# Performance work log

Hardware: AMD Instinct MI355X
Metric: run time of the kernel (lower is better)

Reference implementation:

```python
import jax, jax.numpy as jnp
import numpy as np
import math

HIDDEN = 1024
HEADS = 16
HEAD_DIM = HIDDEN // HEADS
B, S = 2, 2048


def setup_inputs() -> dict:
    key = jax.random.key(0)
    ks = jax.random.split(key, 10)
    std = 1.0 / math.sqrt(HIDDEN)
    mk = lambda k: (jax.random.normal(k, (HIDDEN, HIDDEN), jnp.float32) * std)
    return {
        "hidden_states": jax.random.normal(ks[0], (B, S, HIDDEN), jnp.float32),
        "attention_mask": jnp.zeros((B, 1, 1, S), jnp.float32),
        "wq": mk(ks[1]), "bq": jnp.zeros((HIDDEN,), jnp.float32),
        "wk": mk(ks[2]), "bk": jnp.zeros((HIDDEN,), jnp.float32),
        "wv": mk(ks[3]), "bv": jnp.zeros((HIDDEN,), jnp.float32),
        "wo": mk(ks[4]), "bo": jnp.zeros((HIDDEN,), jnp.float32),
    }


def reference(hidden_states, attention_mask, wq, bq, wk, bk, wv, bv, wo, bo):
    b, s, _ = hidden_states.shape
    scale = math.sqrt(HEAD_DIM)
    # projections (torch Linear: x @ W.T + b); weights stored as [out, in]
    q = hidden_states @ wq.T + bq
    k = hidden_states @ wk.T + bk
    v = hidden_states @ wv.T + bv
    # [B, H, S, D]
    q = q.reshape(b, s, HEADS, HEAD_DIM).transpose(0, 2, 1, 3)
    k = k.reshape(b, s, HEADS, HEAD_DIM).transpose(0, 2, 1, 3)
    v = v.reshape(b, s, HEADS, HEAD_DIM).transpose(0, 2, 1, 3)
    scores = jnp.einsum("bhqd,bhkd->bhqk", q, k) / scale
    scores = scores + attention_mask  # broadcast [B,1,1,S]
    weights = jax.nn.softmax(scores, axis=-1)  # dropout = identity (eval)
    out = jnp.einsum("bhqk,bhkd->bhqd", weights, v)
    out = out.transpose(0, 2, 1, 3).reshape(b, s, HIDDEN)
    out = out @ wo.T + bo
    return out
```

## Files before the change

### kernel.cpp

```cpp
#include <hip/hip_runtime.h>
#include <hip/hip_bf16.h>

typedef __bf16 bf16_t;
typedef __bf16 bf16x8 __attribute__((ext_vector_type(8)));
typedef _Float16 f16x4 __attribute__((ext_vector_type(4)));
typedef _Float16 f16x8 __attribute__((ext_vector_type(8)));
typedef float f32x4 __attribute__((ext_vector_type(4)));

#define SEQ    2048
#define NH     16
#define HD     64
#define HIDDEN 1024
#define LOG2E  1.44269504f
#define CSTR   41

#if __has_builtin(__builtin_amdgcn_exp2f)
#define EXP2F(x) __builtin_amdgcn_exp2f(x)
#else
#define EXP2F(x) exp2f(x)
#endif

__device__ __forceinline__ bf16_t to_bf16(float f) { return (bf16_t)f; }

__device__ __forceinline__ void async16(const void* g, void* l) {
    __builtin_amdgcn_global_load_lds((const __attribute__((address_space(1))) void*)g,
                                     (__attribute__((address_space(3))) void*)l, 16, 0, 0);
}

__global__ __launch_bounds__(256) void cvt_kernel(
    const float* __restrict__ s0, bf16_t* __restrict__ d0, int c0,
    const float* __restrict__ s1, bf16_t* __restrict__ d1, int c1,
    const float* __restrict__ s2, bf16_t* __restrict__ d2, int c2,
    const float* __restrict__ s3, bf16_t* __restrict__ d3, int c3,
    const float* __restrict__ s4, bf16_t* __restrict__ d4, int c4,
    const float* __restrict__ s5, float* __restrict__ d5)
{
    int blk = blockIdx.x;
    const float* s; bf16_t* d;
    if (blk < c0)              { s = s0; d = d0; }
    else if ((blk -= c0) < c1) { s = s1; d = d1; }
    else if ((blk -= c1) < c2) { s = s2; d = d2; }
    else if ((blk -= c2) < c3) { s = s3; d = d3; }
    else if ((blk -= c3) < c4) { s = s4; d = d4; }
    else {
        blk -= c4;
        const size_t base = (size_t)blk * 2048 + threadIdx.x * 8;
        float4 a = *(const float4*)&s5[base];
        float4 b = *(const float4*)&s5[base + 4];
        a.x *= LOG2E; a.y *= LOG2E; a.z *= LOG2E; a.w *= LOG2E;
        b.x *= LOG2E; b.y *= LOG2E; b.z *= LOG2E; b.w *= LOG2E;
        *(float4*)&d5[base] = a;
        *(float4*)&d5[base + 4] = b;
        return;
    }
    const size_t base = (size_t)blk * 2048 + threadIdx.x * 8;
    const float4 a = *(const float4*)&s[base];
    const float4 b = *(const float4*)&s[base + 4];
    bf16x8 o;
    o[0] = (bf16_t)a.x; o[1] = (bf16_t)a.y; o[2] = (bf16_t)a.z; o[3] = (bf16_t)a.w;
    o[4] = (bf16_t)b.x; o[5] = (bf16_t)b.y; o[6] = (bf16_t)b.z; o[7] = (bf16_t)b.w;
    *(bf16x8*)&d[base] = o;
}

__global__ __launch_bounds__(256, 3) void qkv_kernel(
    const bf16_t* __restrict__ X,
    const bf16_t* __restrict__ wq, const bf16_t* __restrict__ wk, const bf16_t* __restrict__ wv,
    const float* __restrict__ bq, const float* __restrict__ bk, const float* __restrict__ bv,
    bf16_t* __restrict__ qws, bf16_t* __restrict__ kws, _Float16* __restrict__ vws)
{
    __shared__ __align__(16) bf16_t Sh[16384];
    const int z = blockIdx.z;
    const bf16_t* Wsel = (z == 0) ? wq : (z == 1) ? wk : wv;
    const float*  bsel = (z == 0) ? bq : (z == 1) ? bk : bv;
    const int m0 = blockIdx.y * 128, n0 = blockIdx.x * 128;

    const int t = threadIdx.x, lane = t & 63, w = t >> 6;
    const int w0 = w & 1, w1 = w >> 1, l15 = lane & 15, q4 = lane >> 4;

    f32x4 acc[4][4];
#pragma unroll
    for (int i = 0; i < 4; i++)
#pragma unroll
        for (int j = 0; j < 4; j++) acc[i][j] = f32x4{0.f, 0.f, 0.f, 0.f};

    auto stage = [&](int kt, int buf) {
#pragma unroll
        for (int j = 0; j < 2; j++) {
            const int s = j * 256 + t;
            const int row = s >> 2, c = (s & 3) ^ (row & 3);
            const int lb = buf * 8192 + (j * 256 + w * 64) * 8;
            async16(&X[(size_t)(m0 + row) * HIDDEN + kt + c * 8], &Sh[lb]);
            async16(&Wsel[(size_t)(n0 + row) * HIDDEN + kt + c * 8], &Sh[lb + 4096]);
        }
    };
    stage(0, 0);

    for (int it = 0; it < 32; it++) {
        const int cur = it & 1;
        __syncthreads();
        if (it < 31) stage((it + 1) * 32, cur ^ 1);
        const bf16_t* As = &Sh[cur * 8192];
        const bf16_t* Bs = &Sh[cur * 8192 + 4096];
        bf16x8 af[4];
#pragma unroll
        for (int ti = 0; ti < 4; ti++) {
            const int ra = w0 * 64 + ti * 16 + l15;
            af[ti] = *(const bf16x8*)&As[ra * 32 + (q4 ^ (ra & 3)) * 8];
        }
#pragma unroll
        for (int tj = 0; tj < 4; tj++) {
            const int rb = w1 * 64 + tj * 16 + l15;
            const bf16x8 bfr = *(const bf16x8*)&Bs[rb * 32 + (q4 ^ (rb & 3)) * 8];
#pragma unroll
            for (int ti = 0; ti < 4; ti++)
                acc[ti][tj] = __builtin_amdgcn_mfma_f32_16x16x32_bf16(af[ti], bfr, acc[ti][tj], 0, 0, 0);
        }
    }
    __syncthreads();

    if (z < 2) {
#pragma unroll
        for (int tj = 0; tj < 4; tj++) {
            const int n = w1 * 64 + tj * 16 + l15;
            const float bb = bsel[n0 + n];
            const int ch = (n >> 3), sub = n & 7;
#pragma unroll
            for (int ti = 0; ti < 4; ti++)
#pragma unroll
                for (int r = 0; r < 4; r++) {
                    const int m = w0 * 64 + ti * 16 + q4 * 4 + r;
                    Sh[m * 128 + ((ch ^ (m & 15)) << 3) + sub] = to_bf16(acc[ti][tj][r] + bb);
                }
        }
        __syncthreads();
        bf16_t* dst = (z == 0) ? qws : kws;
#pragma unroll
        for (int i = 0; i < 8; i++) {
            const int g = i * 256 + t;
            const int row = g >> 4, c = g & 15;
            const bf16x8 vv = *(const bf16x8*)&Sh[row * 128 + ((c ^ (row & 15)) << 3)];
            *(bf16x8*)&dst[(size_t)(m0 + row) * HIDDEN + n0 + c * 8] = vv;
        }
    } else {
        _Float16* Vt = (_Float16*)Sh;
#pragma unroll
        for (int tj = 0; tj < 4; tj++) {
            const int n = w1 * 64 + tj * 16 + l15;
            const float bb = bsel[n0 + n];
#pragma unroll
            for (int ti = 0; ti < 4; ti++) {
                const int mb = w0 * 64 + ti * 16 + q4 * 4;
                f16x4 v;
#pragma unroll
                for (int r = 0; r < 4; r++) v[r] = (_Float16)(acc[ti][tj][r] + bb);
                *(f16x4*)&Vt[n * 128 + (((mb >> 3) ^ (n & 15)) << 3) + (mb & 7)] = v;
            }
        }
        __syncthreads();
        const int b = m0 >> 11, sbase = m0 & (SEQ - 1);
#pragma unroll
        for (int i = 0; i < 8; i++) {
            const int g = i * 256 + t;
            const int row = g >> 4, c = g & 15;
            const int sA = (c >> 2) * 32 + (c & 3) * 4;
            const int sB = sA + 16;
            const f16x4 va = *(const f16x4*)&Vt[row * 128 + (((sA >> 3) ^ (row & 15)) << 3) + (sA & 7)];
            const f16x4 vb = *(const f16x4*)&Vt[row * 128 + (((sB >> 3) ^ (row & 15)) << 3) + (sB & 7)];
            f16x8 vv;
            vv[0] = va[0]; vv[1] = va[1]; vv[2] = va[2]; vv[3] = va[3];
            vv[4] = vb[0]; vv[5] = vb[1]; vv[6] = vb[2]; vv[7] = vb[3];
            const int d = (n0 + row) & 63, hh = (n0 + row) >> 6;
            *(f16x8*)&vws[(((size_t)b * NH + hh) * HD + d) * SEQ + sbase + c * 8] = vv;
        }
    }
}

__global__ __launch_bounds__(256, 4) void attn_kernel(
    const bf16_t* __restrict__ Qw, const bf16_t* __restrict__ Kw,
    const _Float16* __restrict__ Vtw, const float* __restrict__ Msc,
    bf16_t* __restrict__ Ow)
{
    __shared__ __align__(16) bf16_t Tiles[2][2][64 * 64];

    const int t = threadIdx.x, lane = t & 63, w = t >> 6;
    const int l15 = lane & 15, q4 = lane >> 4;
    const int wq = w & 1, kp = w >> 1;
    const int lid = blockIdx.x;
    const int c8 = lid & 7, jx = lid >> 3;
    const int bh = c8 * 4 + (jx >> 5);
    const int q0 = (jx & 31) * 64;
    const int b = bh >> 4, h = bh & 15;

    const bf16_t* Qh = Qw + (size_t)b * SEQ * HIDDEN + h * HD;
    const bf16_t* Kh = Kw + (size_t)b * SEQ * HIDDEN + h * HD;
    const _Float16* Vh = Vtw + (size_t)bh * HD * SEQ;
    const float* Mrow = Msc + (size_t)b * SEQ;

    bf16x8 qf[2][2];
#pragma unroll
    for (int qb = 0; qb < 2; qb++)
#pragma unroll
        for (int ks = 0; ks < 2; ks++)
            qf[qb][ks] = *(const bf16x8*)&Qh[(size_t)(q0 + wq * 32 + qb * 16 + l15) * HIDDEN + ks * 32 + q4 * 8];

    f32x4 oacc[2][4];
#pragma unroll
    for (int qb = 0; qb < 2; qb++)
#pragma unroll
        for (int db = 0; db < 4; db++) oacc[qb][db] = f32x4{0.f, 0.f, 0.f, 0.f};
    f32x4 osum[2];
    osum[0] = f32x4{0.f, 0.f, 0.f, 0.f};
    osum[1] = f32x4{0.f, 0.f, 0.f, 0.f};

    f16x8 vone;
#pragma unroll
    for (int i = 0; i < 8; i++) vone[i] = (_Float16)1.0f;

    int koff[4];
#pragma unroll
    for (int cb = 0; cb < 2; cb++)
#pragma unroll
        for (int ks = 0; ks < 2; ks++) {
            const int rk = kp * 32 + cb * 16 + l15;
            koff[cb * 2 + ks] = rk * 64 + (((ks * 4 + q4) ^ (rk & 7)) << 3);
        }
    int voff[4];
#pragma unroll
    for (int db = 0; db < 4; db++) {
        const int rv = db * 16 + l15;
        voff[db] = rv * 64 + (((kp * 4 + q4) ^ (rv & 7)) << 3);
    }

    const int rs0 = t >> 3, cs0 = (t & 7) ^ (rs0 & 7);
    const int rs1 = 32 + rs0, cs1 = (t & 7) ^ (rs1 & 7);
    const bf16_t*   Kp0 = Kh + (size_t)rs0 * HIDDEN + cs0 * 8;
    const bf16_t*   Kp1 = Kh + (size_t)rs1 * HIDDEN + cs1 * 8;
    const _Float16* Vp0 = Vh + (size_t)rs0 * SEQ + cs0 * 8;
    const _Float16* Vp1 = Vh + (size_t)rs1 * SEQ + cs1 * 8;
    const int db0 = (0 * 256 + w * 64) * 8, db1 = (1 * 256 + w * 64) * 8;

    auto stageKV = [&](int it, int buf) {
        const int kt = it * 64;
        bf16_t*   Kd = &Tiles[buf][0][0];
        _Float16* Vd = (_Float16*)&Tiles[buf][1][0];
        async16(Kp0 + (size_t)kt * HIDDEN, &Kd[db0]);
        async16(Vp0 + kt,                  &Vd[db0]);
        async16(Kp1 + (size_t)kt * HIDDEN, &Kd[db1]);
        async16(Vp1 + kt,                  &Vd[db1]);
    };

    auto iterBody = [&](int it, int buf) {
        __syncthreads();
        if (it < 31) stageKV(it + 1, buf ^ 1);

        const bf16_t*   Ksh = &Tiles[buf][0][0];
        const _Float16* Vsh = (const _Float16*)&Tiles[buf][1][0];

        float4 mv4[2];
#pragma unroll
        for (int cb = 0; cb < 2; cb++)
            mv4[cb] = *(const float4*)&Mrow[it * 64 + kp * 32 + cb * 16 + q4 * 4];

        f32x4 sa[2][2];
#pragma unroll
        for (int qb = 0; qb < 2; qb++)
#pragma unroll
            for (int cb = 0; cb < 2; cb++) sa[qb][cb] = f32x4{0.f, 0.f, 0.f, 0.f};
        __builtin_amdgcn_s_setprio(1);
#pragma unroll
        for (int cb = 0; cb < 2; cb++)
#pragma unroll
            for (int ks = 0; ks < 2; ks++) {
                const bf16x8 kf = *(const bf16x8*)&Ksh[koff[cb * 2 + ks]];
                sa[0][cb] = __builtin_amdgcn_mfma_f32_16x16x32_bf16(kf, qf[0][ks], sa[0][cb], 0, 0, 0);
                sa[1][cb] = __builtin_amdgcn_mfma_f32_16x16x32_bf16(kf, qf[1][ks], sa[1][cb], 0, 0, 0);
            }
        __builtin_amdgcn_s_setprio(0);

        f16x8 pa[2];
#pragma unroll
        for (int cb = 0; cb < 2; cb++) {
            const float4 mv = mv4[cb];
            const float mk[4] = {mv.x, mv.y, mv.z, mv.w};
#pragma unroll
            for (int qb = 0; qb < 2; qb++)
#pragma unroll
                for (int r = 0; r < 4; r++) {
                    const float p = EXP2F(fmaf(sa[qb][cb][r], 0.125f * LOG2E, mk[r]));
                    pa[qb][cb * 4 + r] = (_Float16)p;
                }
        }

        __builtin_amdgcn_s_setprio(1);
#pragma unroll
        for (int db = 0; db < 4; db++) {
            const f16x8 vf = *(const f16x8*)&Vsh[voff[db]];
            oacc[0][db] = __builtin_amdgcn_mfma_f32_16x16x32_f16(pa[0], vf, oacc[0][db], 0, 0, 0);
            oacc[1][db] = __builtin_amdgcn_mfma_f32_16x16x32_f16(pa[1], vf, oacc[1][db], 0, 0, 0);
        }
        osum[0] = __builtin_amdgcn_mfma_f32_16x16x32_f16(pa[0], vone, osum[0], 0, 0, 0);
        osum[1] = __builtin_amdgcn_mfma_f32_16x16x32_f16(pa[1], vone, osum[1], 0, 0, 0);
        __builtin_amdgcn_s_setprio(0);
    };

    stageKV(0, 0);
#pragma unroll 1
    for (int it2 = 0; it2 < 16; it2++) {
        iterBody(it2 * 2, 0);
        iterBody(it2 * 2 + 1, 1);
    }
    __syncthreads();

    float* Cb = (float*)&Tiles[0][0][0];
    const int crow = (wq * 64 + lane) * CSTR;
    if (kp == 1) {
#pragma unroll
        for (int qb = 0; qb < 2; qb++) {
#pragma unroll
            for (int db = 0; db < 4; db++)
                *(f32x4*)&Cb[crow + (qb * 4 + db) * 4] = oacc[qb][db];
            *(f32x4*)&Cb[crow + 32 + qb * 4] = osum[qb];
        }
    }
    __syncthreads();
    if (kp == 0) {
#pragma unroll
        for (int qb = 0; qb < 2; qb++) {
#pragma unroll
            for (int db = 0; db < 4; db++)
                oacc[qb][db] += *(const f32x4*)&Cb[crow + (qb * 4 + db) * 4];
            osum[qb] += *(const f32x4*)&Cb[crow + 32 + qb * 4];
        }
#pragma unroll
        for (int qb = 0; qb < 2; qb++) {
            float inv[4];
#pragma unroll
            for (int r = 0; r < 4; r++) inv[r] = 1.f / osum[qb][r];
#pragma unroll
            for (int r = 0; r < 4; r++) {
                const int srow = q0 + wq * 32 + qb * 16 + q4 * 4 + r;
#pragma unroll
                for (int db = 0; db < 4; db++)
                    Ow[((size_t)b * SEQ + srow) * HIDDEN + h * HD + db * 16 + l15] =
                        to_bf16(oacc[qb][db][r] * inv[r]);
            }
        }
    }
}

__global__ __launch_bounds__(256, 2) void oproj_kernel(
    const bf16_t* __restrict__ A, const bf16_t* __restrict__ Wo,
    const float* __restrict__ bo, float* __restrict__ Out)
{
    __shared__ __align__(16) bf16_t Sh[12288];
    const int m0 = blockIdx.y * 64, n0 = blockIdx.x * 128;
    const int t = threadIdx.x, lane = t & 63, w = t >> 6;
    const int l15 = lane & 15, q4 = lane >> 4;

    f32x4 acc[4][2];
#pragma unroll
    for (int i = 0; i < 4; i++)
#pragma unroll
        for (int j = 0; j < 2; j++) acc[i][j] = f32x4{0.f, 0.f, 0.f, 0.f};

    auto stage = [&](int kt, int buf) {
        {
            const int row = t >> 2, c = (t & 3) ^ (row & 3);
            async16(&A[(size_t)(m0 + row) * HIDDEN + kt + c * 8], &Sh[buf * 6144 + w * 64 * 8]);
        }
#pragma unroll
        for (int j = 0; j < 2; j++) {
            const int s = j * 256 + t;
            const int row = s >> 2, c = (s & 3) ^ (row & 3);
            async16(&Wo[(size_t)(n0 + row) * HIDDEN + kt + c * 8],
                    &Sh[buf * 6144 + 2048 + (j * 256 + w * 64) * 8]);
        }
    };
    stage(0, 0);

    for (int it = 0; it < 32; it++) {
        const int cur = it & 1;
        __syncthreads();
        if (it < 31) stage((it + 1) * 32, cur ^ 1);
        const bf16_t* As = &Sh[cur * 6144];
        const bf16_t* Bs = &Sh[cur * 6144 + 2048];
        bf16x8 af[4];
#pragma unroll
        for (int ti = 0; ti < 4; ti++) {
            const int ra = ti * 16 + l15;
            af[ti] = *(const bf16x8*)&As[ra * 32 + (q4 ^ (ra & 3)) * 8];
        }
#pragma unroll
        for (int tj = 0; tj < 2; tj++) {
            const int rb = w * 32 + tj * 16 + l15;
            const bf16x8 bfr = *(const bf16x8*)&Bs[rb * 32 + (q4 ^ (rb & 3)) * 8];
#pragma unroll
            for (int ti = 0; ti < 4; ti++)
                acc[ti][tj] = __builtin_amdgcn_mfma_f32_16x16x32_bf16(bfr, af[ti], acc[ti][tj], 0, 0, 0);
        }
    }

#pragma unroll
    for (int tj = 0; tj < 2; tj++) {
        const int nb4 = n0 + w * 32 + tj * 16 + q4 * 4;
        const float4 bb = *(const float4*)&bo[nb4];
#pragma unroll
        for (int ti = 0; ti < 4; ti++) {
            const int m = m0 + ti * 16 + l15;
            float4 ov;
            ov.x = acc[ti][tj][0] + bb.x;
            ov.y = acc[ti][tj][1] + bb.y;
            ov.z = acc[ti][tj][2] + bb.z;
            ov.w = acc[ti][tj][3] + bb.w;
            *(float4*)&Out[(size_t)m * HIDDEN + nb4] = ov;
        }
    }
}

extern "C" void kernel_launch(void* const* d_in, const int* in_sizes, int n_in,
                              void* d_out, int out_size, void* d_ws, size_t ws_size,
                              hipStream_t stream) {
    const float* X   = (const float*)d_in[0];
    const float* msk = (const float*)d_in[1];
    const float* wq  = (const float*)d_in[2];
    const float* bq  = (const float*)d_in[3];
    const float* wk  = (const float*)d_in[4];
    const float* bk  = (const float*)d_in[5];
    const float* wv  = (const float*)d_in[6];
    const float* bv  = (const float*)d_in[7];
    const float* wo  = (const float*)d_in[8];
    const float* bo  = (const float*)d_in[9];
    float* out = (float*)d_out;

    const size_t NELT = (size_t)2 * SEQ * HIDDEN;
    const size_t WELT = (size_t)HIDDEN * HIDDEN;
    bf16_t*    xbf = (bf16_t*)d_ws;
    bf16_t*    qws = xbf + NELT;
    bf16_t*    kws = qws + NELT;
    _Float16*  vws = (_Float16*)(kws + NELT);
    bf16_t*    aws = xbf;
    bf16_t*    wqb = (bf16_t*)d_out;
    bf16_t*    wkb = wqb + WELT;
    bf16_t*    wvb = wkb + WELT;
    bf16_t*    wob = wvb + WELT;
    float*     mws = (float*)(wob + WELT);

    cvt_kernel<<<dim3(2048 + 4 * 512 + 2), dim3(256), 0, stream>>>(
        X, xbf, 2048, wq, wqb, 512, wk, wkb, 512, wv, wvb, 512, wo, wob, 512,
        msk, mws);
    qkv_kernel<<<dim3(8, 32, 3), dim3(256), 0, stream>>>(
        xbf, wqb, wkb, wvb, bq, bk, bv, qws, kws, vws);
    attn_kernel<<<dim3(1024), dim3(256), 0, stream>>>(qws, kws, vws, mws, aws);
    oproj_kernel<<<dim3(8, 64), dim3(256), 0, stream>>>(aws, wob, bo, out);
}
```

Baseline: 195.5 us.

## Software-pipeline attention loop: overlap PV of previous tile with QK of current

Restructures the attention main loop so the P·V MFMAs for the previous key tile are issued together with the Q·K MFMAs for the current tile, with the exp/softmax step moved to the end of each iteration. K is double-buffered and V is triple-buffered in a flat LDS array using rotating offsets. The aim is to let the exp work overlap matrix-core work and cut MFMA idle time between dependent phases. In exchange, LDS use rises from 32KB to 40KB per block, which may reduce occupancy under the 4-blocks-per-CU launch bound, and register pressure increases because the probability fragments stay live across the iteration.

```diff
diff --git a/kernel.cpp b/kernel.cpp
--- a/kernel.cpp
+++ b/kernel.cpp
@@ -180,7 +180,8 @@
     const _Float16* __restrict__ Vtw, const float* __restrict__ Msc,
     bf16_t* __restrict__ Ow)
 {
-    __shared__ __align__(16) bf16_t Tiles[2][2][64 * 64];
+    __shared__ __align__(16) bf16_t Tl[5 * 4096];
+    const int TS = 4096, VB = 2 * 4096;
 
     const int t = threadIdx.x, lane = t & 63, w = t >> 6;
     const int l15 = lane & 15, q4 = lane >> 4;
@@ -237,50 +238,35 @@
     const bf16_t*   Kp1 = Kh + (size_t)rs1 * HIDDEN + cs1 * 8;
     const _Float16* Vp0 = Vh + (size_t)rs0 * SEQ + cs0 * 8;
     const _Float16* Vp1 = Vh + (size_t)rs1 * SEQ + cs1 * 8;
-    const int db0 = (0 * 256 + w * 64) * 8, db1 = (1 * 256 + w * 64) * 8;
-
-    auto stageKV = [&](int it, int buf) {
+    const int sl0 = (w * 64) * 8, sl1 = (256 + w * 64) * 8;
+
+    auto stageKV = [&](int it, int kb, int vb) {
         const int kt = it * 64;
-        bf16_t*   Kd = &Tiles[buf][0][0];
-        _Float16* Vd = (_Float16*)&Tiles[buf][1][0];
-        async16(Kp0 + (size_t)kt * HIDDEN, &Kd[db0]);
-        async16(Vp0 + kt,                  &Vd[db0]);
-        async16(Kp1 + (size_t)kt * HIDDEN, &Kd[db1]);
-        async16(Vp1 + kt,                  &Vd[db1]);
-    };
-
-    auto iterBody = [&](int it, int buf) {
-        __syncthreads();
-        if (it < 31) stageKV(it + 1, buf ^ 1);
-
-        const bf16_t*   Ksh = &Tiles[buf][0][0];
-        const _Float16* Vsh = (const _Float16*)&Tiles[buf][1][0];
-
-        float4 mv4[2];
+        async16(Kp0 + (size_t)kt * HIDDEN, &Tl[kb + sl0]);
+        async16(Vp0 + kt,                  &Tl[vb + sl0]);
+        async16(Kp1 + (size_t)kt * HIDDEN, &Tl[kb + sl1]);
+        async16(Vp1 + kt,                  &Tl[vb + sl1]);
+    };
+
+    auto doQK = [&](int kb, f32x4 sa[2][2]) {
+#pragma unroll
+        for (int qb = 0; qb < 2; qb++)
+#pragma unroll
+            for (int cb = 0; cb < 2; cb++) sa[qb][cb] = f32x4{0.f, 0.f, 0.f, 0.f};
 #pragma unroll
         for (int cb = 0; cb < 2; cb++)
-            mv4[cb] = *(const float4*)&Mrow[it * 64 + kp * 32 + cb * 16 + q4 * 4];
-
-        f32x4 sa[2][2];
-#pragma unroll
-        for (int qb = 0; qb < 2; qb++)
-#pragma unroll
-            for (int cb = 0; cb < 2; cb++) sa[qb][cb] = f32x4{0.f, 0.f, 0.f, 0.f};
-        __builtin_amdgcn_s_setprio(1);
-#pragma unroll
-        for (int cb = 0; cb < 2; cb++)
 #pragma unroll
             for (int ks = 0; ks < 2; ks++) {
-                const bf16x8 kf = *(const bf16x8*)&Ksh[koff[cb * 2 + ks]];
+                const bf16x8 kf = *(const bf16x8*)&Tl[kb + koff[cb * 2 + ks]];
                 sa[0][cb] = __builtin_amdgcn_mfma_f32_16x16x32_bf16(kf, qf[0][ks], sa[0][cb], 0, 0, 0);
                 sa[1][cb] = __builtin_amdgcn_mfma_f32_16x16x32_bf16(kf, qf[1][ks], sa[1][cb], 0, 0, 0);
             }
-        __builtin_amdgcn_s_setprio(0);
-
-        f16x8 pa[2];
+    };
+
+    auto doEXP = [&](int it, f32x4 sa[2][2], f16x8 pa[2]) {
 #pragma unroll
         for (int cb = 0; cb < 2; cb++) {
-            const float4 mv = mv4[cb];
+            const float4 mv = *(const float4*)&Mrow[it * 64 + kp * 32 + cb * 16 + q4 * 4];
             const float mk[4] = {mv.x, mv.y, mv.z, mv.w};
 #pragma unroll
             for (int qb = 0; qb < 2; qb++)
@@ -290,28 +276,55 @@
                     pa[qb][cb * 4 + r] = (_Float16)p;
                 }
         }
-
-        __builtin_amdgcn_s_setprio(1);
+    };
+
+    auto doPV = [&](int vb, const f16x8 pa[2]) {
 #pragma unroll
         for (int db = 0; db < 4; db++) {
-            const f16x8 vf = *(const f16x8*)&Vsh[voff[db]];
+            const f16x8 vf = *(const f16x8*)&Tl[vb + voff[db]];
             oacc[0][db] = __builtin_amdgcn_mfma_f32_16x16x32_f16(pa[0], vf, oacc[0][db], 0, 0, 0);
             oacc[1][db] = __builtin_amdgcn_mfma_f32_16x16x32_f16(pa[1], vf, oacc[1][db], 0, 0, 0);
         }
         osum[0] = __builtin_amdgcn_mfma_f32_16x16x32_f16(pa[0], vone, osum[0], 0, 0, 0);
         osum[1] = __builtin_amdgcn_mfma_f32_16x16x32_f16(pa[1], vone, osum[1], 0, 0, 0);
+    };
+
+    stageKV(0, 0, VB);
+    __syncthreads();
+    stageKV(1, TS, VB + TS);
+    f16x8 paP[2];
+    {
+        f32x4 sa[2][2];
+        __builtin_amdgcn_s_setprio(1);
+        doQK(0, sa);
         __builtin_amdgcn_s_setprio(0);
-    };
-
-    stageKV(0, 0);
+        doEXP(0, sa, paP);
+    }
+
+    int kbC = TS, kbN = 0;
+    int vbP = VB, vbC = VB + TS, vbN = VB + 2 * TS;
+
 #pragma unroll 1
-    for (int it2 = 0; it2 < 16; it2++) {
-        iterBody(it2 * 2, 0);
-        iterBody(it2 * 2 + 1, 1);
-    }
+    for (int it = 1; it < 32; ++it) {
+        __syncthreads();
+        if (it < 31) stageKV(it + 1, kbN, vbN);
+        __builtin_amdgcn_s_setprio(1);
+        doPV(vbP, paP);
+        f32x4 sa[2][2];
+        doQK(kbC, sa);
+        __builtin_amdgcn_s_setprio(0);
+        f16x8 paC[2];
+        doEXP(it, sa, paC);
+        paP[0] = paC[0]; paP[1] = paC[1];
+        const int tk = kbC; kbC = kbN; kbN = tk;
+        const int tv = vbP; vbP = vbC; vbC = vbN; vbN = tv;
+    }
+    __builtin_amdgcn_s_setprio(1);
+    doPV(vbP, paP);
+    __builtin_amdgcn_s_setprio(0);
     __syncthreads();
 
-    float* Cb = (float*)&Tiles[0][0][0];
+    float* Cb = (float*)&Tl[0];
     const int crow = (wq * 64 + lane) * CSTR;
     if (kp == 1) {
 #pragma unroll
```

New measurement: 187.5 us. -4.1%, faster.
